# Optimization experiments

Hardware: AMD Instinct MI355X
Metric: run time of the kernel (lower is better)

## Reference

```python
import jax, jax.numpy as jnp
import numpy as np
import math

N_EMBD = 1024
BATCH = 8
T = 2048
INIT_DECAY = 0.95


def setup_inputs() -> dict:
    key = jax.random.key(0)
    k1, k2 = jax.random.split(key)
    raw_init = math.log(INIT_DECAY / (1.0 - INIT_DECAY))
    x = jax.random.normal(k1, (BATCH, T, N_EMBD), dtype=jnp.float32)
    raw_a = jnp.full((N_EMBD,), raw_init, dtype=jnp.float32)
    B = jax.random.normal(k2, (N_EMBD, N_EMBD), dtype=jnp.float32) * 0.01
    h0 = jnp.zeros((BATCH, N_EMBD), dtype=jnp.float32)
    return {"x": x, "raw_a": raw_a, "B": B, "h0": h0}


def reference(x, raw_a, B, h0):
    # a: [H] diagonal decay in (0,1)
    a = jax.nn.sigmoid(raw_a)
    # Precompute the dense projection for all timesteps at once: u[b,t,h] = x[b,t,:] @ B.T
    u = jnp.einsum('btc,hc->bth', x, B)
    # Diagonal linear recurrence h_t = a * h_{t-1} + u_t via lax.scan over time.
    u_t_first = jnp.swapaxes(u, 0, 1)  # [T, B, H]

    def step(h, u_t):
        h = h * a + u_t
        return h, h

    _, ys = jax.lax.scan(step, h0, u_t_first)  # ys: [T, B, H]
    return jnp.swapaxes(ys, 0, 1)  # [B, T, H]
```

## Files before the change

kernel.cpp:

```cpp
#include <hip/hip_runtime.h>
#include <hip/hip_bf16.h>

using bf16 = __hip_bfloat16;
typedef __attribute__((ext_vector_type(8))) short frag8;
typedef __attribute__((ext_vector_type(4))) float f32x4;

constexpr int   H_   = 1024;
constexpr int   B_   = 8;
constexpr int   T_   = 2048;
constexpr int   K_   = H_;
constexpr int   N_   = H_;
constexpr long  M_   = (long)B_ * T_;
constexpr int   SEG  = 64;
constexpr int   TSEG = T_ / SEG;
constexpr int   NCH  = B_ * H_;
constexpr int   NVC  = NCH / 4;

__device__ __forceinline__ unsigned short f2bf(float f) {
  bf16 b = __float2bfloat16(f);
  return *reinterpret_cast<unsigned short*>(&b);
}

__device__ __forceinline__ float4 fma4(float4 h, float4 a, float4 v) {
  float4 r;
  r.x = fmaf(h.x, a.x, v.x);
  r.y = fmaf(h.y, a.y, v.y);
  r.z = fmaf(h.z, a.z, v.z);
  r.w = fmaf(h.w, a.w, v.w);
  return r;
}

__global__ __launch_bounds__(256) void k_convert(const float* __restrict__ x,
                                                 const float* __restrict__ Bm,
                                                 const float* __restrict__ raw,
                                                 unsigned short* __restrict__ xb,
                                                 unsigned short* __restrict__ Bb,
                                                 float* __restrict__ a_sig) {
  const long NX4 = (M_ * K_) / 4;
  const long NB4 = ((long)N_ * K_) / 4;
  long t = (long)blockIdx.x * 256 + threadIdx.x;
  const float* src; unsigned short* dst;
  if (t < NX4) { src = x; dst = xb; }
  else if (t < NX4 + NB4) { t -= NX4; src = Bm; dst = Bb; }
  else {
    long q = t - NX4 - NB4;
    if (q >= H_ / 4) return;
    float4 v = *reinterpret_cast<const float4*>(raw + q * 4);
    float4 o;
    o.x = 1.0f / (1.0f + expf(-v.x));
    o.y = 1.0f / (1.0f + expf(-v.y));
    o.z = 1.0f / (1.0f + expf(-v.z));
    o.w = 1.0f / (1.0f + expf(-v.w));
    *reinterpret_cast<float4*>(a_sig + q * 4) = o;
    return;
  }
  long i = t * 4;
  float4 v = *reinterpret_cast<const float4*>(src + i);
  short4 o;
  o.x = (short)f2bf(v.x);
  o.y = (short)f2bf(v.y);
  o.z = (short)f2bf(v.z);
  o.w = (short)f2bf(v.w);
  *reinterpret_cast<short4*>(dst + i) = o;
}

__global__ __launch_bounds__(256) void k_gemm(const unsigned short* __restrict__ A,
                                              const unsigned short* __restrict__ Bb,
                                              float* __restrict__ C) {
  constexpr int BK = 32;
  __shared__ __align__(16) unsigned short lA[128 * BK];
  __shared__ __align__(16) unsigned short lB[128 * BK];
  const int tid  = threadIdx.x;
  const int lane = tid & 63;
  const int wave = tid >> 6;
  const long m0 = (long)blockIdx.x * 128;
  const long n0 = (long)blockIdx.y * 128;
  const int wm = (wave >> 1) * 64;
  const int wn = (wave & 1) * 64;
  const int quad = lane >> 4;
  const int l16  = lane & 15;

  const unsigned short* gA = A  + (m0 + (tid >> 2)) * K_ + (tid & 3) * 8;
  const unsigned short* gB = Bb + (n0 + (tid >> 2)) * K_ + (tid & 3) * 8;
  unsigned short* sA = &lA[(tid & ~63) * 8];
  unsigned short* sB = &lB[(tid & ~63) * 8];

  f32x4 acc[4][4];
  #pragma unroll
  for (int i = 0; i < 4; i++)
    #pragma unroll
    for (int j = 0; j < 4; j++)
      acc[i][j] = f32x4{0.f, 0.f, 0.f, 0.f};

  for (int k0 = 0; k0 < K_; k0 += BK) {
    __builtin_amdgcn_global_load_lds(
        (const __attribute__((address_space(1))) void*)(gA + k0),
        (__attribute__((address_space(3))) void*)sA, 16, 0, 0);
    __builtin_amdgcn_global_load_lds(
        (const __attribute__((address_space(1))) void*)(gA + 64 * K_ + k0),
        (__attribute__((address_space(3))) void*)(sA + 64 * BK), 16, 0, 0);
    __builtin_amdgcn_global_load_lds(
        (const __attribute__((address_space(1))) void*)(gB + k0),
        (__attribute__((address_space(3))) void*)sB, 16, 0, 0);
    __builtin_amdgcn_global_load_lds(
        (const __attribute__((address_space(1))) void*)(gB + 64 * K_ + k0),
        (__attribute__((address_space(3))) void*)(sB + 64 * BK), 16, 0, 0);
    __syncthreads();

    frag8 af[4], bfr[4];
    #pragma unroll
    for (int i = 0; i < 4; i++) {
      af[i]  = *reinterpret_cast<const frag8*>(&lA[(wm + i * 16 + l16) * BK + quad * 8]);
      bfr[i] = *reinterpret_cast<const frag8*>(&lB[(wn + i * 16 + l16) * BK + quad * 8]);
    }
    #pragma unroll
    for (int i = 0; i < 4; i++)
      #pragma unroll
      for (int j = 0; j < 4; j++)
        acc[i][j] = __builtin_amdgcn_mfma_f32_16x16x32_bf16(af[i], bfr[j], acc[i][j], 0, 0, 0);
    __syncthreads();
  }

  #pragma unroll
  for (int i = 0; i < 4; i++)
    #pragma unroll
    for (int j = 0; j < 4; j++) {
      long r0 = m0 + wm + i * 16 + quad * 4;
      long c0 = n0 + wn + j * 16 + l16;
      #pragma unroll
      for (int r = 0; r < 4; r++)
        C[(r0 + r) * N_ + c0] = acc[i][j][r];
    }
}

__global__ __launch_bounds__(256) void k_seg_ends(const float* __restrict__ u,
                                                  const float* __restrict__ a_sig,
                                                  float* __restrict__ E) {
  int g = blockIdx.x * 256 + threadIdx.x;
  int vc = g & (NVC - 1);
  int s  = g >> 11;
  int b  = vc >> 8;
  int h4 = (vc & 255) * 4;
  float4 a = *reinterpret_cast<const float4*>(a_sig + h4);
  const float* base = u + (long)b * T_ * H_ + (long)s * TSEG * H_ + h4;
  float4 e = {0.f, 0.f, 0.f, 0.f};
  #pragma unroll
  for (int t0 = 0; t0 < TSEG; t0 += 8) {
    float4 v[8];
    #pragma unroll
    for (int j = 0; j < 8; j++)
      v[j] = *reinterpret_cast<const float4*>(base + (long)(t0 + j) * H_);
    #pragma unroll
    for (int j = 0; j < 8; j++)
      e = fma4(e, a, v[j]);
  }
  *reinterpret_cast<float4*>(E + (long)g * 4) = e;
}

__global__ __launch_bounds__(256) void k_carries(float* __restrict__ EC,
                                                 const float* __restrict__ h0,
                                                 const float* __restrict__ a_sig) {
  int c = blockIdx.x * 256 + threadIdx.x;
  if (c >= NCH) return;
  float a = a_sig[c & (H_ - 1)];
  float aL = a;
  #pragma unroll
  for (int i = 0; i < 5; i++) aL *= aL;
  float carry = h0[c];
  #pragma unroll
  for (int s0 = 0; s0 < SEG; s0 += 8) {
    float e[8];
    #pragma unroll
    for (int j = 0; j < 8; j++) e[j] = EC[(long)(s0 + j) * NCH + c];
    #pragma unroll
    for (int j = 0; j < 8; j++) {
      EC[(long)(s0 + j) * NCH + c] = carry;
      carry = fmaf(aL, carry, e[j]);
    }
  }
}

__global__ __launch_bounds__(256) void k_scan(float* __restrict__ u,
                                              const float* __restrict__ Cc,
                                              const float* __restrict__ a_sig) {
  int g = blockIdx.x * 256 + threadIdx.x;
  int vc = g & (NVC - 1);
  int s  = g >> 11;
  int b  = vc >> 8;
  int h4 = (vc & 255) * 4;
  float4 a = *reinterpret_cast<const float4*>(a_sig + h4);
  float4 hs = *reinterpret_cast<const float4*>(Cc + (long)g * 4);
  float* base = u + (long)b * T_ * H_ + (long)s * TSEG * H_ + h4;

  float4 v0[8], v1[8];
  #pragma unroll
  for (int j = 0; j < 8; j++)
    v0[j] = *reinterpret_cast<const float4*>(base + (long)j * H_);

  #pragma unroll
  for (int t0 = 0; t0 < TSEG; t0 += 8) {
    const bool odd = (t0 >> 3) & 1;
    float4* cur = odd ? v1 : v0;
    float4* nxt = odd ? v0 : v1;
    if (t0 + 8 < TSEG) {
      #pragma unroll
      for (int j = 0; j < 8; j++)
        nxt[j] = *reinterpret_cast<const float4*>(base + (long)(t0 + 8 + j) * H_);
    }
    #pragma unroll
    for (int j = 0; j < 8; j++) {
      hs = fma4(hs, a, cur[j]);
      cur[j] = hs;
    }
    #pragma unroll
    for (int j = 0; j < 8; j++)
      *reinterpret_cast<float4*>(base + (long)(t0 + j) * H_) = cur[j];
  }
}

extern "C" void kernel_launch(void* const* d_in, const int* in_sizes, int n_in,
                              void* d_out, int out_size, void* d_ws, size_t ws_size,
                              hipStream_t stream) {
  const float* x    = (const float*)d_in[0];
  const float* rawa = (const float*)d_in[1];
  const float* Bm   = (const float*)d_in[2];
  const float* h0   = (const float*)d_in[3];
  float* u = (float*)d_out;

  char* w = (char*)d_ws;
  unsigned short* xb = (unsigned short*)w;
  unsigned short* Bb = (unsigned short*)(w + 33554432);
  float* a_sig = (float*)(w + 33554432 + 2097152);
  float* EC    = (float*)(w + 33554432 + 2097152 + 4096);

  hipLaunchKernelGGL(k_convert, dim3(17409), dim3(256), 0, stream, x, Bm, rawa, xb, Bb, a_sig);
  hipLaunchKernelGGL(k_gemm, dim3(128, 8), dim3(256), 0, stream, xb, Bb, u);
  hipLaunchKernelGGL(k_seg_ends, dim3(NVC * SEG / 256), dim3(256), 0, stream, u, a_sig, EC);
  hipLaunchKernelGGL(k_carries, dim3(NCH / 256), dim3(256), 0, stream, EC, h0, a_sig);
  hipLaunchKernelGGL(k_scan, dim3(NVC * SEG / 256), dim3(256), 0, stream, u, EC, a_sig);
}
```

Measured before the change: 201.8 us.

## Rewrite GEMM as 256x256 tile, 8-wave double-buffered pipelined kernel

```diff
diff --git a/kernel.cpp b/kernel.cpp
--- a/kernel.cpp
+++ b/kernel.cpp
@@ -64,69 +64,94 @@
   *reinterpret_cast<short4*>(dst + i) = o;
 }
 
-__global__ __launch_bounds__(256) void k_gemm(const unsigned short* __restrict__ A,
-                                              const unsigned short* __restrict__ Bb,
-                                              float* __restrict__ C) {
-  constexpr int BK = 32;
-  __shared__ __align__(16) unsigned short lA[128 * BK];
-  __shared__ __align__(16) unsigned short lB[128 * BK];
+#define MEMBAR asm volatile("" ::: "memory")
+#define BARR do { MEMBAR; __builtin_amdgcn_s_barrier(); MEMBAR; } while (0)
+#define VMW(n) asm volatile("s_waitcnt vmcnt(" #n ")" ::: "memory")
+#define GLDS(SRC, DST) __builtin_amdgcn_global_load_lds( \
+    (const __attribute__((address_space(1))) void*)(SRC), \
+    (__attribute__((address_space(3))) void*)(DST), 16, 0, 0)
+
+__global__ __launch_bounds__(512, 2) void k_gemm(const unsigned short* __restrict__ A,
+                                                 const unsigned short* __restrict__ Bb,
+                                                 float* __restrict__ C) {
+  __shared__ __align__(16) unsigned short lA[32768];
+  __shared__ __align__(16) unsigned short lB[32768];
   const int tid  = threadIdx.x;
-  const int lane = tid & 63;
-  const int wave = tid >> 6;
-  const long m0 = (long)blockIdx.x * 128;
-  const long n0 = (long)blockIdx.y * 128;
-  const int wm = (wave >> 1) * 64;
-  const int wn = (wave & 1) * 64;
-  const int quad = lane >> 4;
-  const int l16  = lane & 15;
-
-  const unsigned short* gA = A  + (m0 + (tid >> 2)) * K_ + (tid & 3) * 8;
-  const unsigned short* gB = Bb + (n0 + (tid >> 2)) * K_ + (tid & 3) * 8;
-  unsigned short* sA = &lA[(tid & ~63) * 8];
-  unsigned short* sB = &lB[(tid & ~63) * 8];
-
-  f32x4 acc[4][4];
-  #pragma unroll
-  for (int i = 0; i < 4; i++)
-    #pragma unroll
-    for (int j = 0; j < 4; j++)
-      acc[i][j] = f32x4{0.f, 0.f, 0.f, 0.f};
-
-  for (int k0 = 0; k0 < K_; k0 += BK) {
-    __builtin_amdgcn_global_load_lds(
-        (const __attribute__((address_space(1))) void*)(gA + k0),
-        (__attribute__((address_space(3))) void*)sA, 16, 0, 0);
-    __builtin_amdgcn_global_load_lds(
-        (const __attribute__((address_space(1))) void*)(gA + 64 * K_ + k0),
-        (__attribute__((address_space(3))) void*)(sA + 64 * BK), 16, 0, 0);
-    __builtin_amdgcn_global_load_lds(
-        (const __attribute__((address_space(1))) void*)(gB + k0),
-        (__attribute__((address_space(3))) void*)sB, 16, 0, 0);
-    __builtin_amdgcn_global_load_lds(
-        (const __attribute__((address_space(1))) void*)(gB + 64 * K_ + k0),
-        (__attribute__((address_space(3))) void*)(sB + 64 * BK), 16, 0, 0);
-    __syncthreads();
-
-    frag8 af[4], bfr[4];
-    #pragma unroll
-    for (int i = 0; i < 4; i++) {
-      af[i]  = *reinterpret_cast<const frag8*>(&lA[(wm + i * 16 + l16) * BK + quad * 8]);
-      bfr[i] = *reinterpret_cast<const frag8*>(&lB[(wn + i * 16 + l16) * BK + quad * 8]);
-    }
-    #pragma unroll
-    for (int i = 0; i < 4; i++)
-      #pragma unroll
-      for (int j = 0; j < 4; j++)
-        acc[i][j] = __builtin_amdgcn_mfma_f32_16x16x32_bf16(af[i], bfr[j], acc[i][j], 0, 0, 0);
-    __syncthreads();
-  }
-
-  #pragma unroll
-  for (int i = 0; i < 4; i++)
+  const int wid  = tid >> 6, lane = tid & 63;
+  const int wr   = wid >> 2, wc = wid & 3;
+  const int quad = lane >> 4, l16 = lane & 15;
+  const int bh   = wc >> 1, br = (wc & 1) * 64;
+  const int bid  = blockIdx.x;
+  const int wgid = (bid & 7) * 32 + (bid >> 3);
+  const long m0 = (long)(wgid >> 2) * 256;
+  const long n0 = (long)(wgid & 3) * 256;
+  const unsigned short* gA = A  + (m0 + (tid >> 3)) * K_ + (tid & 7) * 8;
+  const unsigned short* gB = Bb + (n0 + (tid >> 3)) * K_ + (tid & 7) * 8;
+  unsigned short* sAw = lA + wid * 512;
+  unsigned short* sBw = lB + wid * 512;
+
+#define STG_A(d, hf, t) do { \
+    GLDS(gA + ((hf) * 128) * K_ + (t) * 64,      sAw + (d) * 16384 + (hf) * 8192); \
+    GLDS(gA + ((hf) * 128 + 64) * K_ + (t) * 64, sAw + (d) * 16384 + (hf) * 8192 + 4096); } while (0)
+#define STG_B(d, hf, t) do { \
+    GLDS(gB + ((hf) * 128) * K_ + (t) * 64,      sBw + (d) * 16384 + (hf) * 8192); \
+    GLDS(gB + ((hf) * 128 + 64) * K_ + (t) * 64, sBw + (d) * 16384 + (hf) * 8192 + 4096); } while (0)
+
+  f32x4 acc[8][4];
+  #pragma unroll
+  for (int i = 0; i < 8; i++)
+    #pragma unroll
+    for (int j = 0; j < 4; j++) acc[i][j] = f32x4{0.f, 0.f, 0.f, 0.f};
+
+  frag8 aR[4][2];
+  frag8 bR[2][2][2];
+
+#define RD_A(d, ih) do { _Pragma("unroll") \
+    for (int ii = 0; ii < 4; ii++) { \
+      const unsigned short* p = lA + (d) * 16384 + wr * 8192 + (((ih) * 4 + ii) * 16 + l16) * 64 + quad * 8; \
+      aR[ii][0] = *(const frag8*)p; \
+      aR[ii][1] = *(const frag8*)(p + 32); } } while (0)
+#define RD_B(d, jh) do { _Pragma("unroll") \
+    for (int jj = 0; jj < 2; jj++) { \
+      const unsigned short* p = lB + (d) * 16384 + bh * 8192 + (br + ((jh) * 2 + jj) * 16 + l16) * 64 + quad * 8; \
+      bR[jh][jj][0] = *(const frag8*)p; \
+      bR[jh][jj][1] = *(const frag8*)(p + 32); } } while (0)
+#define MMQ(ih, jh) do { __builtin_amdgcn_s_setprio(1); _Pragma("unroll") \
+    for (int ii = 0; ii < 4; ii++) { _Pragma("unroll") \
+      for (int jj = 0; jj < 2; jj++) { \
+        acc[(ih)*4+ii][(jh)*2+jj] = __builtin_amdgcn_mfma_f32_16x16x32_bf16(aR[ii][0], bR[jh][jj][0], acc[(ih)*4+ii][(jh)*2+jj], 0, 0, 0); \
+        acc[(ih)*4+ii][(jh)*2+jj] = __builtin_amdgcn_mfma_f32_16x16x32_bf16(aR[ii][1], bR[jh][jj][1], acc[(ih)*4+ii][(jh)*2+jj], 0, 0, 0); } } \
+    __builtin_amdgcn_s_setprio(0); } while (0)
+
+  STG_A(0, 0, 0); STG_A(0, 1, 0); STG_B(0, 0, 0); STG_B(0, 1, 0); STG_A(1, 0, 1);
+  VMW(2); BARR;
+
+  for (int it = 0; it < 7; ++it) {
+    const int to = 2 * it + 1, te2 = 2 * it + 2, to2 = 2 * it + 3;
+    RD_A(0, 0); RD_B(0, 0); STG_A(1, 1, to);  BARR; MMQ(0, 0);         BARR;
+    RD_B(0, 1);             STG_B(1, 0, to);  BARR; MMQ(0, 1);         BARR;
+    RD_A(0, 1);             STG_B(1, 1, to);  BARR; MMQ(1, 1);         BARR;
+                            STG_A(0, 0, te2); BARR; MMQ(1, 0); VMW(2); BARR;
+    RD_A(1, 0); RD_B(1, 0); STG_A(0, 1, te2); BARR; MMQ(0, 0);         BARR;
+    RD_B(1, 1);             STG_B(0, 0, te2); BARR; MMQ(0, 1);         BARR;
+    RD_A(1, 1);             STG_B(0, 1, te2); BARR; MMQ(1, 1);         BARR;
+                            STG_A(1, 0, to2); BARR; MMQ(1, 0); VMW(2); BARR;
+  }
+  RD_A(0, 0); RD_B(0, 0); STG_A(1, 1, 15); BARR; MMQ(0, 0);         BARR;
+  RD_B(0, 1);             STG_B(1, 0, 15); BARR; MMQ(0, 1);         BARR;
+  RD_A(0, 1);             STG_B(1, 1, 15); BARR; MMQ(1, 1);         BARR;
+                                           BARR; MMQ(1, 0); VMW(0); BARR;
+  RD_A(1, 0); RD_B(1, 0);                  BARR; MMQ(0, 0);         BARR;
+  RD_B(1, 1);                              BARR; MMQ(0, 1);         BARR;
+  RD_A(1, 1);                              BARR; MMQ(1, 1);         BARR;
+  MMQ(1, 0);
+
+  #pragma unroll
+  for (int i = 0; i < 8; i++)
     #pragma unroll
     for (int j = 0; j < 4; j++) {
-      long r0 = m0 + wm + i * 16 + quad * 4;
-      long c0 = n0 + wn + j * 16 + l16;
+      const long r0 = m0 + wr * 128 + i * 16 + quad * 4;
+      const long c0 = n0 + wc * 64 + j * 16 + l16;
       #pragma unroll
       for (int r = 0; r < 4; r++)
         C[(r0 + r) * N_ + c0] = acc[i][j][r];
@@ -234,7 +259,7 @@
   float* EC    = (float*)(w + 33554432 + 2097152 + 4096);
 
   hipLaunchKernelGGL(k_convert, dim3(17409), dim3(256), 0, stream, x, Bm, rawa, xb, Bb, a_sig);
-  hipLaunchKernelGGL(k_gemm, dim3(128, 8), dim3(256), 0, stream, xb, Bb, u);
+  hipLaunchKernelGGL(k_gemm, dim3(256), dim3(512), 0, stream, xb, Bb, u);
   hipLaunchKernelGGL(k_seg_ends, dim3(NVC * SEG / 256), dim3(256), 0, stream, u, a_sig, EC);
   hipLaunchKernelGGL(k_carries, dim3(NCH / 256), dim3(256), 0, stream, EC, h0, a_sig);
   hipLaunchKernelGGL(k_scan, dim3(NVC * SEG / 256), dim3(256), 0, stream, u, EC, a_sig);
```

New measurement: 196.9 us. 1.02x faster.
